# Kernel optimization log

Measured on AMD Instinct MI355X. Metric: run time of the kernel, lower is better.

## Reference

```python
import jax, jax.numpy as jnp
import numpy as np

N_PATCHES = 14
PS = 16            # patch size: 224 / 14
C, H_IMG, W_IMG = 3, 224, 224
HIDDEN = 768
HEADS = 12
DH = HIDDEN // HEADS
BLOCKS = 12
MLP = 4 * HIDDEN
OUT = 1000
SEQ = N_PATCHES ** 2 + 1  # 197
BATCH = 64


def get_positional_embeddings(seq_len, d):
    # sin(i/10000^(j/d)) for even j, cos(i/10000^((j-1)/d)) for odd j
    i = jnp.arange(seq_len, dtype=jnp.float32)[:, None]
    j = jnp.arange(d)[None, :]
    even = (j % 2 == 0)
    expo = jnp.where(even, j, j - 1).astype(jnp.float32) / d
    ang = i / (10000.0 ** expo)
    return jnp.where(even, jnp.sin(ang), jnp.cos(ang))


def layernorm(x, g, b, eps=1e-5):
    mu = x.mean(-1, keepdims=True)
    var = ((x - mu) ** 2).mean(-1, keepdims=True)
    return (x - mu) / jnp.sqrt(var + eps) * g + b


def mhsa(x, qw, qb, kw, kb, vw, vb):
    # x: [B,S,HIDDEN]; per-head linears qw/kw/vw: [H,DH,DH] (torch Linear weight layout)
    B, S, _ = x.shape
    xh = x.reshape(B, S, HEADS, DH)
    q = jnp.einsum('bshd,hed->bshe', xh, qw) + qb
    k = jnp.einsum('bshd,hed->bshe', xh, kw) + kb
    v = jnp.einsum('bshd,hed->bshe', xh, vw) + vb
    scores = jnp.einsum('bshe,bthe->bhst', q, k) / jnp.sqrt(jnp.float32(DH))
    attn = jax.nn.softmax(scores, axis=-1)
    out = jnp.einsum('bhst,bthe->bshe', attn, v)
    return out.reshape(B, S, HIDDEN)


def vit_block(x, p):
    ln1_g, ln1_b, qw, qb, kw, kb, vw, vb, ln2_g, ln2_b, w1, b1, w2, b2 = p
    x = x + mhsa(layernorm(x, ln1_g, ln1_b), qw, qb, kw, kb, vw, vb)
    h = layernorm(x, ln2_g, ln2_b)
    h = jax.nn.gelu(h @ w1.T + b1, approximate=False) @ w2.T + b2
    return x + h


def patchify(images):
    # [N,C,H,W] -> [N, n_patches^2, C*PS*PS], channel-major within each patch
    n = images.shape[0]
    x = images.reshape(n, C, N_PATCHES, PS, N_PATCHES, PS)
    x = x.transpose(0, 2, 4, 1, 3, 5)  # n, pi, pj, c, ps, ps
    return x.reshape(n, N_PATCHES * N_PATCHES, C * PS * PS)


def setup_inputs() -> dict:
    key = jax.random.key(0)
    ks = jax.random.split(key, 20)
    s = 0.02
    return {
        'images': jax.random.normal(ks[0], (BATCH, C, H_IMG, W_IMG), jnp.float32),
        'mapper_w': jax.random.normal(ks[1], (HIDDEN, C * PS * PS), jnp.float32) * s,
        'mapper_b': jnp.zeros((HIDDEN,), jnp.float32),
        'cls_token': jax.random.uniform(ks[2], (1, HIDDEN), jnp.float32),
        'ln1_g': jnp.ones((BLOCKS, HIDDEN), jnp.float32),
        'ln1_b': jnp.zeros((BLOCKS, HIDDEN), jnp.float32),
        'qw': jax.random.normal(ks[3], (BLOCKS, HEADS, DH, DH), jnp.float32) * s,
        'qb': jnp.zeros((BLOCKS, HEADS, DH), jnp.float32),
        'kw': jax.random.normal(ks[4], (BLOCKS, HEADS, DH, DH), jnp.float32) * s,
        'kb': jnp.zeros((BLOCKS, HEADS, DH), jnp.float32),
        'vw': jax.random.normal(ks[5], (BLOCKS, HEADS, DH, DH), jnp.float32) * s,
        'vb': jnp.zeros((BLOCKS, HEADS, DH), jnp.float32),
        'ln2_g': jnp.ones((BLOCKS, HIDDEN), jnp.float32),
        'ln2_b': jnp.zeros((BLOCKS, HIDDEN), jnp.float32),
        'w1': jax.random.normal(ks[6], (BLOCKS, MLP, HIDDEN), jnp.float32) * s,
        'b1': jnp.zeros((BLOCKS, MLP), jnp.float32),
        'w2': jax.random.normal(ks[7], (BLOCKS, HIDDEN, MLP), jnp.float32) * s,
        'b2': jnp.zeros((BLOCKS, HIDDEN), jnp.float32),
        'head_w': jax.random.normal(ks[8], (OUT, HIDDEN), jnp.float32) * s,
        'head_b': jnp.zeros((OUT,), jnp.float32),
    }


def reference(images, mapper_w, mapper_b, cls_token, ln1_g, ln1_b, qw, qb, kw, kb,
              vw, vb, ln2_g, ln2_b, w1, b1, w2, b2, head_w, head_b):
    n = images.shape[0]
    patches = patchify(images)
    tokens = patches @ mapper_w.T + mapper_b                      # [B, 196, HIDDEN]
    cls = jnp.broadcast_to(cls_token[None], (n, 1, HIDDEN))
    tokens = jnp.concatenate([cls, tokens], axis=1)               # [B, 197, HIDDEN]
    out = tokens + get_positional_embeddings(SEQ, HIDDEN)[None]

    stacked = (ln1_g, ln1_b, qw, qb, kw, kb, vw, vb, ln2_g, ln2_b, w1, b1, w2, b2)

    def step(x, p):
        return vit_block(x, p), None

    out, _ = jax.lax.scan(step, out, stacked)
    cls_out = out[:, 0]                                           # [B, HIDDEN]
    return jax.nn.softmax(cls_out @ head_w.T + head_b, axis=-1)
```

## Files before the change

### kernel.cpp

```cpp
#include <hip/hip_runtime.h>
#include <cstdint>
#include <cstddef>
#include <cstdio>

using u16 = unsigned short;
using u32 = unsigned int;

typedef __attribute__((ext_vector_type(8))) __bf16 bf16x8;
typedef __attribute__((ext_vector_type(4))) float f32x4;

struct alignas(16) U128 { u32 w[4]; };
struct alignas(16) F4   { float x[4]; };
struct alignas(8)  US4  { u16 h[4]; };

#define DEVFN static __device__ __forceinline__

DEVFN u16 f2bf(float x) {
  union { float f; u32 u; } v; v.f = x;
  u32 r = v.u + 0x7fffu + ((v.u >> 16) & 1u);
  return (u16)(r >> 16);
}

DEVFN bf16x8 ld16(const u16* p) { return __builtin_bit_cast(bf16x8, *(const U128*)p); }

DEVFN f32x4 mfma16(bf16x8 a, bf16x8 b, f32x4 c) {
  return __builtin_amdgcn_mfma_f32_16x16x32_bf16(a, b, c, 0, 0, 0);
}

DEVFN void gload_lds16(const u16* g, u16* l) {
  __builtin_amdgcn_global_load_lds(
      (const __attribute__((address_space(1))) void*)g,
      (__attribute__((address_space(3))) void*)l, 16, 0, 0);
}

DEVFN float gelu(float x) {
  float z = fabsf(x) * 0.70710678118f;
  float t = __builtin_amdgcn_rcpf(1.f + 0.3275911f * z);
  float p = t * (0.254829592f + t * (-0.284496736f + t * (1.421413741f +
            t * (-1.453152027f + t * 1.061405429f))));
  float e = __expf(-z * z);
  float erfz = 1.f - p * e;
  erfz = copysignf(erfz, x);
  return 0.5f * x * (1.f + erfz);
}

DEVFN void remap_bid(int bid, int Mb, int Nb, int& bm, int& bn) {
  const int ngrp  = Mb >> 3;
  const int per   = Nb << 3;
  const int nfull = ngrp * per;
  if (bid < nfull) {
    const int bmg = bid / per;
    const int rem = bid - bmg * per;
    bn = rem >> 3;
    bm = (bmg << 3) + (rem & 7);
  } else {
    const int r = bid - nfull;
    const int q = r / Nb;
    bm = (ngrp << 3) + q;
    bn = r - q * Nb;
  }
}

constexpr int SEQL   = 197;
constexpr int NB     = 64;
constexpr int NH     = 12;
constexpr int MROWS  = NB * SEQL;
constexpr int MPAD   = 12672;
constexpr int MPAD2  = 12800;
constexpr int MPATCH = NB * 196;
constexpr int SP     = 208;
constexpr int SP2    = 224;
constexpr int BHN    = NB * NH;

constexpr size_t OFF_X    = 0;
constexpr size_t OFF_ALN  = OFF_X    + (size_t)MPAD * 768 * 4;
constexpr size_t OFF_H    = OFF_ALN  + (size_t)MPAD2 * 768 * 2;
constexpr size_t OFF_WQKV = OFF_H    + (size_t)MPAD2 * 3072 * 2;
constexpr size_t OFF_W1   = OFF_WQKV + (size_t)2304 * 128 * 2;
constexpr size_t OFF_W2   = OFF_W1   + (size_t)3072 * 768 * 2;
constexpr size_t OFF_WMAP = OFF_W2   + (size_t)3072 * 768 * 2;
constexpr size_t OFF_Q    = OFF_WMAP + (size_t)768 * 768 * 2;
constexpr size_t OFF_K    = OFF_Q    + (size_t)BHN * SP * 64 * 2;
constexpr size_t OFF_VT   = OFF_K    + (size_t)BHN * SP * 64 * 2;
constexpr size_t OFF_PAT  = OFF_VT   + (size_t)BHN * 64 * SP2 * 2;
constexpr size_t OFF_POS  = OFF_PAT  + (size_t)MPATCH * 768 * 2;
constexpr size_t WS_NEED  = OFF_POS  + (size_t)SEQL * 768 * 4;

__global__ void zero_kernel(u32* __restrict__ p, long n) {
  long i = (long)blockIdx.x * 256 + threadIdx.x;
  long stride = (long)gridDim.x * 256;
  for (; i < n; i += stride) p[i] = 0u;
}

__global__ void cvt_kernel(const float* __restrict__ src, u16* __restrict__ dst, int n) {
  int i = blockIdx.x * 256 + threadIdx.x;
  if (i < n) dst[i] = f2bf(src[i]);
}

__global__ void pos_kernel(float* __restrict__ pos) {
  int i = blockIdx.x * 256 + threadIdx.x;
  if (i >= SEQL * 768) return;
  int s = i / 768, j = i - s * 768;
  float expo = (float)(j & ~1) * (1.0f / 768.0f);
  float ang  = (float)s * expf(-expo * logf(10000.0f));
  pos[i] = (j & 1) ? cosf(ang) : sinf(ang);
}

__global__ void cls_kernel(const float* __restrict__ cls, const float* __restrict__ pos,
                           float* __restrict__ X) {
  int b = blockIdx.x;
  for (int c = threadIdx.x; c < 768; c += 256)
    X[(size_t)b * SEQL * 768 + c] = cls[c] + pos[c];
}

__global__ void patchify_kernel(const float* __restrict__ img, u16* __restrict__ out) {
  int i = blockIdx.x * 256 + threadIdx.x;
  if (i >= MPATCH * 768) return;
  int m = i / 768, k = i - m * 768;
  int b = m / 196, p = m - b * 196;
  int py = p / 14, px = p - py * 14;
  int c = k >> 8, rem = k & 255, iy = rem >> 4, ix = rem & 15;
  float v = img[(((size_t)b * 3 + c) * 224 + py * 16 + iy) * 224 + px * 16 + ix];
  out[i] = f2bf(v);
}

__global__ void build_wqkv2(const float* __restrict__ qw, const float* __restrict__ kw,
                            const float* __restrict__ vw, u16* __restrict__ W, int blk) {
  int i = blockIdx.x * 256 + threadIdx.x;
  if (i >= 2304 * 128) return;
  int n = i >> 7, kk = i & 127;
  int p = n / 768, ef = n - p * 768;
  int h = ef >> 6, e = ef & 63;
  float v = 0.f;
  if ((kk >> 6) == (h & 1)) {
    int d = kk & 63;
    const float* w = (p == 0) ? qw : (p == 1) ? kw : vw;
    v = w[(((size_t)blk * NH + h) * 64 + e) * 64 + d];
  }
  W[i] = f2bf(v);
}

__global__ __launch_bounds__(256) void ln_kernel(const float* __restrict__ X,
    const float* __restrict__ g, const float* __restrict__ b, u16* __restrict__ out) {
  int row  = blockIdx.x * 4 + (threadIdx.x >> 6);
  int lane = threadIdx.x & 63;
  const float* x = X + (size_t)row * 768 + lane * 12;
  F4 a0 = *(const F4*)(x);
  F4 a1 = *(const F4*)(x + 4);
  F4 a2 = *(const F4*)(x + 8);
  float v[12];
  #pragma unroll
  for (int j = 0; j < 4; ++j) { v[j] = a0.x[j]; v[4 + j] = a1.x[j]; v[8 + j] = a2.x[j]; }
  float s = 0.f, q = 0.f;
  #pragma unroll
  for (int j = 0; j < 12; ++j) { s += v[j]; q += v[j] * v[j]; }
  #pragma unroll
  for (int d = 1; d < 64; d <<= 1) { s += __shfl_xor(s, d); q += __shfl_xor(q, d); }
  float mu  = s * (1.f / 768.f);
  float var = q * (1.f / 768.f) - mu * mu;
  float rs  = rsqrtf(var + 1e-5f);
  const float* gp = g + lane * 12;
  const float* bp = b + lane * 12;
  u16* op = out + (size_t)row * 768 + lane * 12;
  u16 o[12];
  #pragma unroll
  for (int j = 0; j < 12; ++j) o[j] = f2bf((v[j] - mu) * rs * gp[j] + bp[j]);
  #pragma unroll
  for (int c = 0; c < 3; ++c) {
    US4 w; w.h[0] = o[c*4]; w.h[1] = o[c*4+1]; w.h[2] = o[c*4+2]; w.h[3] = o[c*4+3];
    *(US4*)(op + c * 4) = w;
  }
}

enum { EPI_PATCH = 0, EPI_QKV = 1, EPI_GELU = 2, EPI_RESID = 3 };

template<int EPI>
__global__ __launch_bounds__(256, 3) void gemm128(
    const u16* __restrict__ A, const u16* __restrict__ B, int K, int lda, int ldb,
    int Mb, int Nb,
    const float* __restrict__ e0, const float* __restrict__ e1, const float* __restrict__ e2,
    float* __restrict__ f0, const float* __restrict__ f1,
    u16* __restrict__ o0, u16* __restrict__ o1, u16* __restrict__ o2) {
  __shared__ u16 Ab[3][128 * 32];
  __shared__ u16 Bb[3][128 * 32];
  const int tid  = threadIdx.x;
  const int wave = tid >> 6, lane = tid & 63;
  int bm, bn;
  remap_bid(blockIdx.x, Mb, Nb, bm, bn);
  const int fr = lane & 15, fg = lane >> 4;
  if constexpr (EPI == EPI_QKV) A += (bn % 6) * 128;
  const int srow = wave * 16 + (lane >> 2);
  const int gcol = ((lane & 3) ^ ((lane >> 3) & 3)) * 8;
  const u16* gA = A + (size_t)(bm * 128 + srow) * lda + gcol;
  const u16* gB = B + (size_t)(bn * 128 + srow) * ldb + gcol;
  const int wm = (wave >> 1) * 64, wn = (wave & 1) * 64;
  const int sl = (fg ^ ((fr >> 1) & 3)) * 8;
  const int nt = K >> 5;

  auto STAGE = [&](int c, int t) {
    gload_lds16(gA + t * 32,                    &Ab[c][0] + wave * 512);
    gload_lds16(gA + t * 32 + (size_t)64 * lda, &Ab[c][0] + wave * 512 + 2048);
    gload_lds16(gB + t * 32,                    &Bb[c][0] + wave * 512);
    gload_lds16(gB + t * 32 + (size_t)64 * ldb, &Bb[c][0] + wave * 512 + 2048);
  };

  f32x4 acc[4][4] = {};
  STAGE(0, 0);
  if (nt > 1) STAGE(1, 1);
  int bi = 0;
  for (int t = 0; t < nt; ++t) {
    if (t + 1 < nt) asm volatile("s_waitcnt vmcnt(4)" ::: "memory");
    else            asm volatile("s_waitcnt vmcnt(0)" ::: "memory");
    __builtin_amdgcn_s_barrier();
    if (t + 2 < nt) { int si = bi + 2; if (si >= 3) si -= 3; STAGE(si, t + 2); }
    const u16* ab   = &Ab[bi][0];
    const u16* bbuf = &Bb[bi][0];
    bf16x8 af[4], bfv[4];
    #pragma unroll
    for (int i = 0; i < 4; ++i) af[i]  = ld16(ab + (wm + i * 16 + fr) * 32 + sl);
    #pragma unroll
    for (int j = 0; j < 4; ++j) bfv[j] = ld16(bbuf + (wn + j * 16 + fr) * 32 + sl);
    __builtin_amdgcn_s_setprio(1);
    #pragma unroll
    for (int i = 0; i < 4; ++i)
      #pragma unroll
      for (int j = 0; j < 4; ++j)
        acc[i][j] = mfma16(af[i], bfv[j], acc[i][j]);
    __builtin_amdgcn_s_setprio(0);
    bi = (bi + 1 == 3) ? 0 : bi + 1;
  }

  #pragma unroll
  for (int i = 0; i < 4; ++i) {
    #pragma unroll
    for (int r = 0; r < 4; ++r) {
      const int m = bm * 128 + wm + i * 16 + fg * 4 + r;
      if constexpr (EPI == EPI_PATCH) {
        const int bb = m / 196;
        const int s  = m - bb * 196 + 1;
        float* xrow = f0 + ((size_t)bb * SEQL + s) * 768;
        const float* prow = f1 + (size_t)s * 768;
        #pragma unroll
        for (int j = 0; j < 4; ++j) {
          const int n = bn * 128 + wn + j * 16 + fr;
          xrow[n] = acc[i][j][r] + e0[n] + prow[n];
        }
      } else if constexpr (EPI == EPI_QKV) {
        if (m < MROWS) {
          const int bb = m / 197;
          const int s  = m - bb * 197;
          #pragma unroll
          for (int j = 0; j < 4; ++j) {
            const int n = bn * 128 + wn + j * 16 + fr;
            const int p = n / 768;
            const int ef = n - p * 768;
            const int h = ef >> 6, e = ef & 63;
            const size_t bh = (size_t)bb * NH + h;
            if (p == 0)      o0[(bh * SP + s) * 64 + e] = f2bf((acc[i][j][r] + e0[ef]) * 0.125f);
            else if (p == 1) o1[(bh * SP + s) * 64 + e] = f2bf(acc[i][j][r] + e1[ef]);
            else             o2[(bh * 64 + e) * SP2 + s] = f2bf(acc[i][j][r] + e2[ef]);
          }
        }
      } else if constexpr (EPI == EPI_GELU) {
        u16* hrow = o0 + (size_t)m * 3072;
        #pragma unroll
        for (int j = 0; j < 4; ++j) {
          const int n = bn * 128 + wn + j * 16 + fr;
          hrow[n] = f2bf(gelu(acc[i][j][r] + e0[n]));
        }
      } else {
        if (m < MROWS) {
          float* xrow = f0 + (size_t)m * 768;
          #pragma unroll
          for (int j = 0; j < 4; ++j) {
            const int n = bn * 128 + wn + j * 16 + fr;
            xrow[n] += acc[i][j][r] + e0[n];
          }
        }
      }
    }
  }
}

__global__ __launch_bounds__(256) void attn_kernel(const u16* __restrict__ Q,
    const u16* __restrict__ Km, const u16* __restrict__ Vt, float* __restrict__ X) {
  __shared__ u16  P[4][16 * SP2];
  __shared__ float sums[4][16];
  const int bh = blockIdx.x;
  const int b = bh / NH, h = bh - b * NH;
  const int wave = threadIdx.x >> 6, lane = threadIdx.x & 63;
  const int fr = lane & 15, fg = lane >> 4;
  const u16* Qb = Q  + (size_t)bh * SP * 64;
  const u16* Kb = Km + (size_t)bh * SP * 64;
  const u16* Vb = Vt + (size_t)bh * 64 * SP2;
  u16* Pl = &P[wave][0];
  for (int qt = wave; qt < 13; qt += 4) {
    const int s0 = qt * 16;
    bf16x8 qf0 = ld16(Qb + (size_t)(s0 + fr) * 64 + fg * 8);
    bf16x8 qf1 = ld16(Qb + (size_t)(s0 + fr) * 64 + 32 + fg * 8);
    f32x4 sc[13];
    #pragma unroll
    for (int tf = 0; tf < 13; ++tf) {
      f32x4 a = {0.f, 0.f, 0.f, 0.f};
      bf16x8 k0 = ld16(Kb + (size_t)(tf * 16 + fr) * 64 + fg * 8);
      bf16x8 k1 = ld16(Kb + (size_t)(tf * 16 + fr) * 64 + 32 + fg * 8);
      a = mfma16(qf0, k0, a);
      a = mfma16(qf1, k1, a);
      sc[tf] = a;
    }
    float mx[4] = {-3e38f, -3e38f, -3e38f, -3e38f};
    #pragma unroll
    for (int tf = 0; tf < 13; ++tf) {
      const bool ok = (tf * 16 + fr) < 197;
      #pragma unroll
      for (int r = 0; r < 4; ++r) {
        float v = ok ? sc[tf][r] : -3e38f;
        sc[tf][r] = v;
        mx[r] = fmaxf(mx[r], v);
      }
    }
    #pragma unroll
    for (int r = 0; r < 4; ++r)
      #pragma unroll
      for (int d = 1; d < 16; d <<= 1) mx[r] = fmaxf(mx[r], __shfl_xor(mx[r], d));
    float sm[4] = {0.f, 0.f, 0.f, 0.f};
    #pragma unroll
    for (int tf = 0; tf < 13; ++tf) {
      #pragma unroll
      for (int r = 0; r < 4; ++r) {
        float e = __expf(sc[tf][r] - mx[r]);
        sm[r] += e;
        Pl[(fg * 4 + r) * SP2 + tf * 16 + fr] = f2bf(e);
      }
    }
    #pragma unroll
    for (int r = 0; r < 4; ++r) {
      #pragma unroll
      for (int d = 1; d < 16; d <<= 1) sm[r] += __shfl_xor(sm[r], d);
      if (fr == 0) sums[wave][fg * 4 + r] = sm[r];
    }
    #pragma unroll
    for (int r = 0; r < 4; ++r) Pl[(fg * 4 + r) * SP2 + 208 + fr] = 0;
    f32x4 o[4] = {};
    #pragma unroll
    for (int ks = 0; ks < 7; ++ks) {
      bf16x8 pf = ld16(Pl + fr * SP2 + ks * 32 + fg * 8);
      #pragma unroll
      for (int ef = 0; ef < 4; ++ef) {
        bf16x8 vf = ld16(Vb + (size_t)(ef * 16 + fr) * SP2 + ks * 32 + fg * 8);
        o[ef] = mfma16(vf, pf, o[ef]);
      }
    }
    const float inv = 1.f / sums[wave][fr];
    const int s = s0 + fr;
    if (s < 197) {
      float* xp = X + ((size_t)b * SEQL + s) * 768 + h * 64;
      #pragma unroll
      for (int ef = 0; ef < 4; ++ef)
        #pragma unroll
        for (int r = 0; r < 4; ++r)
          xp[ef * 16 + fg * 4 + r] += o[ef][r] * inv;
    }
  }
}

__global__ __launch_bounds__(256) void head_kernel(const float* __restrict__ X,
    const float* __restrict__ hw, const float* __restrict__ hb, float* __restrict__ out) {
  __shared__ float xr[768];
  __shared__ float lg[1000];
  __shared__ float red[8];
  const int b = blockIdx.x, tid = threadIdx.x;
  for (int c = tid; c < 768; c += 256) xr[c] = X[(size_t)b * SEQL * 768 + c];
  __syncthreads();
  for (int n = tid; n < 1000; n += 256) {
    const F4* w4 = (const F4*)(hw + (size_t)n * 768);
    const F4* x4 = (const F4*)xr;
    float acc = hb[n];
    for (int k = 0; k < 192; ++k) {
      F4 w = w4[k]; F4 xv = x4[k];
      acc += w.x[0] * xv.x[0] + w.x[1] * xv.x[1] + w.x[2] * xv.x[2] + w.x[3] * xv.x[3];
    }
    lg[n] = acc;
  }
  __syncthreads();
  float m = -3e38f;
  for (int n = tid; n < 1000; n += 256) m = fmaxf(m, lg[n]);
  #pragma unroll
  for (int d = 1; d < 64; d <<= 1) m = fmaxf(m, __shfl_xor(m, d));
  if ((tid & 63) == 0) red[tid >> 6] = m;
  __syncthreads();
  m = fmaxf(fmaxf(red[0], red[1]), fmaxf(red[2], red[3]));
  float s = 0.f;
  for (int n = tid; n < 1000; n += 256) s += expf(lg[n] - m);
  #pragma unroll
  for (int d = 1; d < 64; d <<= 1) s += __shfl_xor(s, d);
  if ((tid & 63) == 0) red[4 + (tid >> 6)] = s;
  __syncthreads();
  s = red[4] + red[5] + red[6] + red[7];
  const float inv = 1.f / s;
  for (int n = tid; n < 1000; n += 256) out[(size_t)b * 1000 + n] = expf(lg[n] - m) * inv;
}

extern "C" void kernel_launch(void* const* d_in, const int* in_sizes, int n_in,
                              void* d_out, int out_size, void* d_ws, size_t ws_size,
                              hipStream_t stream) {
  (void)in_sizes; (void)n_in; (void)out_size;
  if (ws_size < WS_NEED) { printf("ws too small: %zu < %zu\n", ws_size, WS_NEED); return; }

  const float* images   = (const float*)d_in[0];
  const float* mapper_w = (const float*)d_in[1];
  const float* mapper_b = (const float*)d_in[2];
  const float* cls_tok  = (const float*)d_in[3];
  const float* ln1_g    = (const float*)d_in[4];
  const float* ln1_b    = (const float*)d_in[5];
  const float* qw       = (const float*)d_in[6];
  const float* qb       = (const float*)d_in[7];
  const float* kw       = (const float*)d_in[8];
  const float* kb       = (const float*)d_in[9];
  const float* vw       = (const float*)d_in[10];
  const float* vb       = (const float*)d_in[11];
  const float* ln2_g    = (const float*)d_in[12];
  const float* ln2_b    = (const float*)d_in[13];
  const float* w1       = (const float*)d_in[14];
  const float* b1       = (const float*)d_in[15];
  const float* w2       = (const float*)d_in[16];
  const float* b2       = (const float*)d_in[17];
  const float* head_w   = (const float*)d_in[18];
  const float* head_b   = (const float*)d_in[19];

  char* ws = (char*)d_ws;
  float* X    = (float*)(ws + OFF_X);
  u16*  Aln   = (u16*)(ws + OFF_ALN);
  u16*  Hb    = (u16*)(ws + OFF_H);
  u16*  Wqkv  = (u16*)(ws + OFF_WQKV);
  u16*  W1b   = (u16*)(ws + OFF_W1);
  u16*  W2b   = (u16*)(ws + OFF_W2);
  u16*  Wmap  = (u16*)(ws + OFF_WMAP);
  u16*  Qb    = (u16*)(ws + OFF_Q);
  u16*  Kb    = (u16*)(ws + OFF_K);
  u16*  Vtb   = (u16*)(ws + OFF_VT);
  u16*  Pat   = (u16*)(ws + OFF_PAT);
  float* Pos  = (float*)(ws + OFF_POS);

  zero_kernel<<<2048, 256, 0, stream>>>((u32*)Qb,  (long)(BHN * SP * 64 / 2));
  zero_kernel<<<2048, 256, 0, stream>>>((u32*)Kb,  (long)(BHN * SP * 64 / 2));
  zero_kernel<<<2048, 256, 0, stream>>>((u32*)Vtb, (long)(BHN * 64 * SP2 / 2));
  zero_kernel<<<64,   256, 0, stream>>>((u32*)(X + (size_t)MROWS * 768), (long)((MPAD - MROWS) * 768));

  pos_kernel<<<(SEQL * 768 + 255) / 256, 256, 0, stream>>>(Pos);
  cvt_kernel<<<(768 * 768 + 255) / 256, 256, 0, stream>>>(mapper_w, Wmap, 768 * 768);
  patchify_kernel<<<(MPATCH * 768 + 255) / 256, 256, 0, stream>>>(images, Pat);
  cls_kernel<<<NB, 256, 0, stream>>>(cls_tok, Pos, X);

  gemm128<EPI_PATCH><<<(MPATCH / 128) * (768 / 128), 256, 0, stream>>>(
      Pat, Wmap, 768, 768, 768, MPATCH / 128, 768 / 128,
      mapper_b, nullptr, nullptr, X, Pos, nullptr, nullptr, nullptr);

  for (int blk = 0; blk < 12; ++blk) {
    ln_kernel<<<MPAD / 4, 256, 0, stream>>>(X, ln1_g + blk * 768, ln1_b + blk * 768, Aln);
    build_wqkv2<<<(2304 * 128 + 255) / 256, 256, 0, stream>>>(qw, kw, vw, Wqkv, blk);
    gemm128<EPI_QKV><<<(MPAD / 128) * (2304 / 128), 256, 0, stream>>>(
        Aln, Wqkv, 128, 768, 128, MPAD / 128, 2304 / 128,
        qb + blk * 768, kb + blk * 768, vb + blk * 768,
        nullptr, nullptr, Qb, Kb, Vtb);
    attn_kernel<<<BHN, 256, 0, stream>>>(Qb, Kb, Vtb, X);
    ln_kernel<<<MPAD / 4, 256, 0, stream>>>(X, ln2_g + blk * 768, ln2_b + blk * 768, Aln);
    cvt_kernel<<<(3072 * 768 + 255) / 256, 256, 0, stream>>>(w1 + (size_t)blk * 3072 * 768, W1b, 3072 * 768);
    gemm128<EPI_GELU><<<(MPAD / 128) * (3072 / 128), 256, 0, stream>>>(
        Aln, W1b, 768, 768, 768, MPAD / 128, 3072 / 128,
        b1 + blk * 3072, nullptr, nullptr, nullptr, nullptr, Hb, nullptr, nullptr);
    cvt_kernel<<<(3072 * 768 + 255) / 256, 256, 0, stream>>>(w2 + (size_t)blk * 768 * 3072, W2b, 768 * 3072);
    gemm128<EPI_RESID><<<(MPAD / 128) * (768 / 128), 256, 0, stream>>>(
        Hb, W2b, 3072, 3072, 3072, MPAD / 128, 768 / 128,
        b2 + blk * 768, nullptr, nullptr, X, nullptr, nullptr, nullptr, nullptr);
  }

  head_kernel<<<NB, 256, 0, stream>>>(X, head_w, head_b, (float*)d_out);
}
```

Measured before the change: 4.441 ms.

## Fuse weight conversions, add dedicated QKV GEMM, stage K in LDS for attention

Merges the per-block QKV weight build and the two MLP weight bf16 conversions into one prep kernel, which removes two launches per block. The QKV projection moves to a dedicated kernel that loads its whole K=128 slice into four LDS buffers at once instead of running the pipelined generic GEMM loop. The attention kernel now copies each head's K matrix into padded LDS once, so the 13 query tiles no longer each re-read it from global memory. The extra LDS and the launch bound of 2 may lower occupancy.

```diff
diff --git a/kernel.cpp b/kernel.cpp
--- a/kernel.cpp
+++ b/kernel.cpp
@@ -124,20 +124,32 @@
   out[i] = f2bf(v);
 }
 
-__global__ void build_wqkv2(const float* __restrict__ qw, const float* __restrict__ kw,
-                            const float* __restrict__ vw, u16* __restrict__ W, int blk) {
+__global__ void prep_kernel(const float* __restrict__ qw, const float* __restrict__ kw,
+                            const float* __restrict__ vw, const float* __restrict__ w1,
+                            const float* __restrict__ w2,
+                            u16* __restrict__ Wqkv, u16* __restrict__ W1b,
+                            u16* __restrict__ W2b, int blk) {
+  const int NQ = 2304 * 128;
+  const int N1 = 3072 * 768;
   int i = blockIdx.x * 256 + threadIdx.x;
-  if (i >= 2304 * 128) return;
-  int n = i >> 7, kk = i & 127;
-  int p = n / 768, ef = n - p * 768;
-  int h = ef >> 6, e = ef & 63;
-  float v = 0.f;
-  if ((kk >> 6) == (h & 1)) {
-    int d = kk & 63;
-    const float* w = (p == 0) ? qw : (p == 1) ? kw : vw;
-    v = w[(((size_t)blk * NH + h) * 64 + e) * 64 + d];
-  }
-  W[i] = f2bf(v);
+  if (i < NQ) {
+    int n = i >> 7, kk = i & 127;
+    int p = n / 768, ef = n - p * 768;
+    int h = ef >> 6, e = ef & 63;
+    float v = 0.f;
+    if ((kk >> 6) == (h & 1)) {
+      int d = kk & 63;
+      const float* w = (p == 0) ? qw : (p == 1) ? kw : vw;
+      v = w[(((size_t)blk * NH + h) * 64 + e) * 64 + d];
+    }
+    Wqkv[i] = f2bf(v);
+  } else if (i < NQ + N1) {
+    int j = i - NQ;
+    W1b[j] = f2bf(w1[(size_t)blk * N1 + j]);
+  } else if (i < NQ + 2 * N1) {
+    int j = i - NQ - N1;
+    W2b[j] = f2bf(w2[(size_t)blk * N1 + j]);
+  }
 }
 
 __global__ __launch_bounds__(256) void ln_kernel(const float* __restrict__ X,
@@ -188,7 +200,6 @@
   int bm, bn;
   remap_bid(blockIdx.x, Mb, Nb, bm, bn);
   const int fr = lane & 15, fg = lane >> 4;
-  if constexpr (EPI == EPI_QKV) A += (bn % 6) * 128;
   const int srow = wave * 16 + (lane >> 2);
   const int gcol = ((lane & 3) ^ ((lane >> 3) & 3)) * 8;
   const u16* gA = A + (size_t)(bm * 128 + srow) * lda + gcol;
@@ -244,22 +255,6 @@
         for (int j = 0; j < 4; ++j) {
           const int n = bn * 128 + wn + j * 16 + fr;
           xrow[n] = acc[i][j][r] + e0[n] + prow[n];
-        }
-      } else if constexpr (EPI == EPI_QKV) {
-        if (m < MROWS) {
-          const int bb = m / 197;
-          const int s  = m - bb * 197;
-          #pragma unroll
-          for (int j = 0; j < 4; ++j) {
-            const int n = bn * 128 + wn + j * 16 + fr;
-            const int p = n / 768;
-            const int ef = n - p * 768;
-            const int h = ef >> 6, e = ef & 63;
-            const size_t bh = (size_t)bb * NH + h;
-            if (p == 0)      o0[(bh * SP + s) * 64 + e] = f2bf((acc[i][j][r] + e0[ef]) * 0.125f);
-            else if (p == 1) o1[(bh * SP + s) * 64 + e] = f2bf(acc[i][j][r] + e1[ef]);
-            else             o2[(bh * 64 + e) * SP2 + s] = f2bf(acc[i][j][r] + e2[ef]);
-          }
         }
       } else if constexpr (EPI == EPI_GELU) {
         u16* hrow = o0 + (size_t)m * 3072;
@@ -282,9 +277,79 @@
   }
 }
 
-__global__ __launch_bounds__(256) void attn_kernel(const u16* __restrict__ Q,
+__global__ __launch_bounds__(256, 2) void qkv_gemm(
+    const u16* __restrict__ A, const u16* __restrict__ B,
+    const float* __restrict__ e0, const float* __restrict__ e1, const float* __restrict__ e2,
+    u16* __restrict__ o0, u16* __restrict__ o1, u16* __restrict__ o2) {
+  __shared__ u16 Ab[4][128 * 32];
+  __shared__ u16 Bb[4][128 * 32];
+  const int tid = threadIdx.x, wave = tid >> 6, lane = tid & 63;
+  int bm, bn;
+  remap_bid(blockIdx.x, MPAD / 128, 18, bm, bn);
+  const int fr = lane & 15, fg = lane >> 4;
+  const u16* Aw = A + (bn % 6) * 128;
+  const int srow = wave * 16 + (lane >> 2);
+  const int gcol = ((lane & 3) ^ ((lane >> 3) & 3)) * 8;
+  const u16* gA = Aw + (size_t)(bm * 128 + srow) * 768 + gcol;
+  const u16* gB = B + (size_t)(bn * 128 + srow) * 128 + gcol;
+  const int wm = (wave >> 1) * 64, wn = (wave & 1) * 64;
+  const int sl = (fg ^ ((fr >> 1) & 3)) * 8;
+
+  #pragma unroll
+  for (int c = 0; c < 4; ++c) {
+    gload_lds16(gA + c * 32,                    &Ab[c][0] + wave * 512);
+    gload_lds16(gA + c * 32 + (size_t)64 * 768, &Ab[c][0] + wave * 512 + 2048);
+    gload_lds16(gB + c * 32,                    &Bb[c][0] + wave * 512);
+    gload_lds16(gB + c * 32 + (size_t)64 * 128, &Bb[c][0] + wave * 512 + 2048);
+  }
+  asm volatile("s_waitcnt vmcnt(0)" ::: "memory");
+  __builtin_amdgcn_s_barrier();
+
+  f32x4 acc[4][4] = {};
+  #pragma unroll
+  for (int c = 0; c < 4; ++c) {
+    bf16x8 af[4], bfv[4];
+    #pragma unroll
+    for (int i = 0; i < 4; ++i) af[i]  = ld16(&Ab[c][0] + (wm + i * 16 + fr) * 32 + sl);
+    #pragma unroll
+    for (int j = 0; j < 4; ++j) bfv[j] = ld16(&Bb[c][0] + (wn + j * 16 + fr) * 32 + sl);
+    __builtin_amdgcn_s_setprio(1);
+    #pragma unroll
+    for (int i = 0; i < 4; ++i)
+      #pragma unroll
+      for (int j = 0; j < 4; ++j)
+        acc[i][j] = mfma16(af[i], bfv[j], acc[i][j]);
+    __builtin_amdgcn_s_setprio(0);
+  }
+
+  #pragma unroll
+  for (int i = 0; i < 4; ++i) {
+    #pragma unroll
+    for (int r = 0; r < 4; ++r) {
+      const int m = bm * 128 + wm + i * 16 + fg * 4 + r;
+      if (m < MROWS) {
+        const int bb = m / 197;
+        const int s  = m - bb * 197;
+        #pragma unroll
+        for (int j = 0; j < 4; ++j) {
+          const int n = bn * 128 + wn + j * 16 + fr;
+          const int p = n / 768;
+          const int ef = n - p * 768;
+          const int h = ef >> 6, e = ef & 63;
+          const size_t bh = (size_t)bb * NH + h;
+          if (p == 0)      o0[(bh * SP + s) * 64 + e] = f2bf((acc[i][j][r] + e0[ef]) * 0.125f);
+          else if (p == 1) o1[(bh * SP + s) * 64 + e] = f2bf(acc[i][j][r] + e1[ef]);
+          else             o2[(bh * 64 + e) * SP2 + s] = f2bf(acc[i][j][r] + e2[ef]);
+        }
+      }
+    }
+  }
+}
+
+__global__ __launch_bounds__(256, 2) void attn_kernel(const u16* __restrict__ Q,
     const u16* __restrict__ Km, const u16* __restrict__ Vt, float* __restrict__ X) {
   __shared__ u16  P[4][16 * SP2];
+  __shared__ u16  Kl[208 * 72];
   __shared__ float sums[4][16];
   const int bh = blockIdx.x;
   const int b = bh / NH, h = bh - b * NH;
@@ -293,6 +358,14 @@
   const u16* Qb = Q  + (size_t)bh * SP * 64;
   const u16* Kb = Km + (size_t)bh * SP * 64;
   const u16* Vb = Vt + (size_t)bh * 64 * SP2;
+  {
+    const int r0 = threadIdx.x >> 2;
+    const int e  = (threadIdx.x & 3) * 16;
+    #pragma unroll
+    for (int rr = r0; rr < 208; rr += 64)
+      *(U128*)(Kl + rr * 72 + e) = *(const U128*)(Kb + (size_t)rr * 64 + e);
+  }
+  __syncthreads();
   u16* Pl = &P[wave][0];
   for (int qt = wave; qt < 13; qt += 4) {
     const int s0 = qt * 16;
@@ -302,8 +375,8 @@
     #pragma unroll
     for (int tf = 0; tf < 13; ++tf) {
       f32x4 a = {0.f, 0.f, 0.f, 0.f};
-      bf16x8 k0 = ld16(Kb + (size_t)(tf * 16 + fr) * 64 + fg * 8);
-      bf16x8 k1 = ld16(Kb + (size_t)(tf * 16 + fr) * 64 + 32 + fg * 8);
+      bf16x8 k0 = ld16(Kl + (tf * 16 + fr) * 72 + fg * 8);
+      bf16x8 k1 = ld16(Kl + (tf * 16 + fr) * 72 + 32 + fg * 8);
       a = mfma16(qf0, k0, a);
       a = mfma16(qf1, k1, a);
       sc[tf] = a;
@@ -456,20 +529,18 @@
       Pat, Wmap, 768, 768, 768, MPATCH / 128, 768 / 128,
       mapper_b, nullptr, nullptr, X, Pos, nullptr, nullptr, nullptr);
 
+  const int PREP_N = 2304 * 128 + 2 * 3072 * 768;
   for (int blk = 0; blk < 12; ++blk) {
     ln_kernel<<<MPAD / 4, 256, 0, stream>>>(X, ln1_g + blk * 768, ln1_b + blk * 768, Aln);
-    build_wqkv2<<<(2304 * 128 + 255) / 256, 256, 0, stream>>>(qw, kw, vw, Wqkv, blk);
-    gemm128<EPI_QKV><<<(MPAD / 128) * (2304 / 128), 256, 0, stream>>>(
-        Aln, Wqkv, 128, 768, 128, MPAD / 128, 2304 / 128,
-        qb + blk * 768, kb + blk * 768, vb + blk * 768,
-        nullptr, nullptr, Qb, Kb, Vtb);
+    prep_kernel<<<(PREP_N + 255) / 256, 256, 0, stream>>>(
+        qw, kw, vw, w1, w2, Wqkv, W1b, W2b, blk);
+    qkv_gemm<<<(MPAD / 128) * 18, 256, 0, stream>>>(
+        Aln, Wqkv, qb + blk * 768, kb + blk * 768, vb + blk * 768, Qb, Kb, Vtb);
     attn_kernel<<<BHN, 256, 0, stream>>>(Qb, Kb, Vtb, X);
     ln_kernel<<<MPAD / 4, 256, 0, stream>>>(X, ln2_g + blk * 768, ln2_b + blk * 768, Aln);
-    cvt_kernel<<<(3072 * 768 + 255) / 256, 256, 0, stream>>>(w1 + (size_t)blk * 3072 * 768, W1b, 3072 * 768);
     gemm128<EPI_GELU><<<(MPAD / 128) * (3072 / 128), 256, 0, stream>>>(
         Aln, W1b, 768, 768, 768, MPAD / 128, 3072 / 128,
         b1 + blk * 3072, nullptr, nullptr, nullptr, nullptr, Hb, nullptr, nullptr);
-    cvt_kernel<<<(3072 * 768 + 255) / 256, 256, 0, stream>>>(w2 + (size_t)blk * 768 * 3072, W2b, 768 * 3072);
     gemm128<EPI_RESID><<<(MPAD / 128) * (768 / 128), 256, 0, stream>>>(
         Hb, W2b, 3072, 3072, 3072, MPAD / 128, 768 / 128,
         b2 + blk * 768, nullptr, nullptr, X, nullptr, nullptr, nullptr, nullptr);
```

After: 4.181 ms. 5.8% less time.
